# Kernel optimization log

Measured on AMD Instinct MI355X. Metric: run time of the kernel, lower is better.

The kernel has to match this reference:

```python
import jax, jax.numpy as jnp
import numpy as np
from jax import lax

D_MODEL = 1024
STATE_DIM = 512
BATCH = 4
SEQ_LEN = 8192


def _cayley_eigenvalues(a_params, n):
    # a_full = [0, a_1..a_half, -a_half-1..., antisymmetric tail]
    half = n // 2
    a_full = jnp.zeros((n,), dtype=a_params.dtype)
    a_full = a_full.at[1:half + 1].set(a_params)
    a_full = a_full.at[half + 1:].set(-a_params[::-1][: n - half - 1])
    a_hat = jnp.fft.fft(a_full)            # complex64
    omega = jnp.imag(a_hat)                # (n,), float32
    ones = jnp.ones_like(omega)
    num = lax.complex(ones, -omega)
    den = lax.complex(ones, omega)
    return num / den                        # (n,), |lambda|=1


def setup_inputs() -> dict:
    key = jax.random.key(0)
    k1, k2, k3, k4 = jax.random.split(key, 4)
    u = jax.random.normal(k1, (BATCH, SEQ_LEN, D_MODEL), dtype=jnp.float32)
    a_params = jax.random.normal(k2, (STATE_DIM // 2,), dtype=jnp.float32) * 0.1
    # torch Linear weights: B.weight (state_dim, d_model), C.weight (d_model, state_dim)
    B_w = jax.random.normal(k3, (STATE_DIM, D_MODEL), dtype=jnp.float32) / np.sqrt(D_MODEL)
    C_w = jax.random.normal(k4, (D_MODEL, STATE_DIM), dtype=jnp.float32) / np.sqrt(STATE_DIM)
    D = jnp.ones((D_MODEL,), dtype=jnp.float32)
    return {"u": u, "a_params": a_params, "B_w": B_w, "C_w": C_w, "D": D}


def reference(u, a_params, B_w, C_w, D):
    batch, seq_len, d = u.shape
    n = B_w.shape[0]
    # 1) input projection: (b, t, n)
    Bu = jnp.einsum("btd,nd->btn", u, B_w)
    # 2) per-channel geometric kernel k_j[t] = lambda_j^t
    eig = _cayley_eigenvalues(a_params, n)                 # (n,) complex64
    t = jnp.arange(seq_len, dtype=jnp.float32)
    kernel = jnp.exp(t[:, None] * jnp.log(eig)[None, :])   # (T, n) complex64
    # 3) causal convolution via FFT with next-pow2(2T) padding
    fft_len = 1
    while fft_len < 2 * seq_len:
        fft_len *= 2
    pad = fft_len - seq_len
    kernel_padded = jnp.pad(kernel, ((0, pad), (0, 0)))
    K_hat = jnp.fft.fft(kernel_padded, axis=0)             # (F, n)
    Bu_padded = jnp.pad(Bu, ((0, 0), (0, pad), (0, 0))).astype(jnp.complex64)
    Bu_hat = jnp.fft.fft(Bu_padded, axis=1)                # (b, F, n)
    h = jnp.fft.ifft(K_hat[None] * Bu_hat, axis=1).real[:, :seq_len, :]
    # 4) output projection + skip
    y = jnp.einsum("btn,dn->btd", h, C_w) + D * u
    return y
```

## Files before the change

kernel.cpp:

```cpp
#include <hip/hip_runtime.h>
#include <cstdint>
#include <cstddef>

#define D_MODEL   1024
#define STATE_DIM 512
#define BATCH     4
#define SEQ_LEN   8192
#define M_TOTAL   (BATCH * SEQ_LEN)

typedef unsigned short ushort_t;
typedef __attribute__((ext_vector_type(8))) __bf16 bf16x8;
typedef __attribute__((ext_vector_type(4))) float  f32x4;


__device__ inline ushort_t f2bf(float f) {
  union { float f; uint32_t u; } v; v.f = f;
  uint32_t u = v.u;
  uint32_t r = (u + 0x7FFFu + ((u >> 16) & 1u)) >> 16;
  return (ushort_t)r;
}

__device__ inline float bf2f(ushort_t b) {
  union { uint32_t u; float f; } v; v.u = ((uint32_t)b) << 16;
  return v.f;
}

__device__ inline void llds16(const void* g, void* l) {
  __builtin_amdgcn_global_load_lds(
      (__attribute__((address_space(1))) void*)(void*)g,
      (__attribute__((address_space(3))) void*)l,
      16, 0, 0);
}


__global__ void convert_f32_bf16(const float* __restrict__ in,
                                 ushort_t* __restrict__ out, int n4) {
  int i = blockIdx.x * blockDim.x + threadIdx.x;
  if (i >= n4) return;
  const float4 v = ((const float4*)in)[i];
  ushort4 o;
  o.x = f2bf(v.x); o.y = f2bf(v.y); o.z = f2bf(v.z); o.w = f2bf(v.w);
  ((ushort4*)out)[i] = o;
}


#define NCHUNK 128
#define CLEN   64
#define SOFF   (BATCH * NCHUNK * STATE_DIM)

__global__ __launch_bounds__(64)
void eigen_kernel(const float* __restrict__ a_params, float* __restrict__ lam) {
  const int k = blockIdx.x;
  const int l = threadIdx.x;
  const float c = 6.283185307179586f / 512.0f;
  float om = 0.f;
#pragma unroll
  for (int s = 0; s < 8; ++s) {
    const int n = s * 64 + l;
    float v = 0.f;
    if (n >= 1 && n <= STATE_DIM / 2)      v = a_params[n - 1];
    else if (n > STATE_DIM / 2)            v = -a_params[STATE_DIM - n];
    const int p = (k * n) & 511;
    om -= v * sinf(c * (float)p);
  }
#pragma unroll
  for (int off = 32; off; off >>= 1) om += __shfl_down(om, off);
  if (l == 0) {
    const float d  = 1.f / (1.f + om * om);
    const float lr = (1.f - om * om) * d;
    const float li = -2.f * om * d;
    double th = atan2((double)li, (double)lr) * (double)CLEN;
    lam[k]        = lr;
    lam[512 + k]  = li;
    lam[1024 + k] = (float)cos(th);
    lam[1536 + k] = (float)sin(th);
  }
}


template <int KDIM, int NDIM, bool OUT_BF16, bool FUSE_SKIP>
__global__ __launch_bounds__(256, 4)
void gemm_bt(const ushort_t* __restrict__ A,
             const ushort_t* __restrict__ Bw,
             void* __restrict__ outv,
             const ushort_t* __restrict__ skip_b,
             const float* __restrict__ Dvec) {
  __shared__ __align__(16) ushort_t smA[2 * 128 * 32];
  __shared__ __align__(16) ushort_t smB[2 * 128 * 32];
  const int tid    = threadIdx.x;
  const int wave   = tid >> 6, lane = tid & 63;
  const int lane16 = lane & 15, quad = lane >> 4;
  const int wm = (wave & 1) * 64, wn = (wave >> 1) * 64;
  const int row0 = blockIdx.x * 128;
  const int col0 = blockIdx.y * 128;

  f32x4 acc[4][4];
#pragma unroll
  for (int i = 0; i < 4; ++i)
#pragma unroll
    for (int j = 0; j < 4; ++j) {
      f32x4 z = {0.f, 0.f, 0.f, 0.f};
      acc[i][j] = z;
    }

  const int s_r0 = tid >> 2;
  const int s_c0 = (tid & 3) ^ ((s_r0 >> 1) & 3);
  const int s_r1 = (256 + tid) >> 2;
  const int s_c1 = (tid & 3) ^ ((s_r1 >> 1) & 3);
  const int o0 = (wave * 64) * 16;
  const int o1 = (256 + wave * 64) * 16;

  const ushort_t* gA0 = A  + (size_t)(row0 + s_r0) * KDIM + s_c0 * 8;
  const ushort_t* gB0 = Bw + (size_t)(col0 + s_r0) * KDIM + s_c0 * 8;
  const ushort_t* gA1 = A  + (size_t)(row0 + s_r1) * KDIM + s_c1 * 8;
  const ushort_t* gB1 = Bw + (size_t)(col0 + s_r1) * KDIM + s_c1 * 8;

#define STAGE(k0, buf)                                                   \
  do {                                                                   \
    char* bA = (char*)(smA + (buf) * (128 * 32));                        \
    char* bB = (char*)(smB + (buf) * (128 * 32));                        \
    llds16(gA0 + (k0), bA + o0);                                         \
    llds16(gB0 + (k0), bB + o0);                                         \
    llds16(gA1 + (k0), bA + o1);                                         \
    llds16(gB1 + (k0), bB + o1);                                         \
  } while (0)

  STAGE(0, 0);
  __syncthreads();

  constexpr int NIT = KDIM / 32;
  int cur = 0;
#pragma unroll 2
  for (int it = 0; it < NIT; ++it) {
    if (it + 1 < NIT) STAGE((it + 1) * 32, cur ^ 1);

    const ushort_t* sA = smA + cur * (128 * 32);
    const ushort_t* sB = smB + cur * (128 * 32);
    bf16x8 af[4], bfr[4];
#pragma unroll
    for (int mi = 0; mi < 4; ++mi) {
      const int m = wm + mi * 16 + lane16;
      const int pc = quad ^ ((m >> 1) & 3);
      af[mi] = *(const bf16x8*)(sA + (m * 4 + pc) * 8);
    }
#pragma unroll
    for (int ni = 0; ni < 4; ++ni) {
      const int n = wn + ni * 16 + lane16;
      const int pc = quad ^ ((n >> 1) & 3);
      bfr[ni] = *(const bf16x8*)(sB + (n * 4 + pc) * 8);
    }
#pragma unroll
    for (int mi = 0; mi < 4; ++mi)
#pragma unroll
      for (int ni = 0; ni < 4; ++ni)
        acc[mi][ni] = __builtin_amdgcn_mfma_f32_16x16x32_bf16(
            af[mi], bfr[ni], acc[mi][ni], 0, 0, 0);

    __syncthreads();
    cur ^= 1;
  }
#undef STAGE

#pragma unroll
  for (int mi = 0; mi < 4; ++mi) {
#pragma unroll
    for (int ni = 0; ni < 4; ++ni) {
      const int row = row0 + wm + mi * 16 + quad * 4;
      const int col = col0 + wn + ni * 16 + lane16;
      float dv = 0.f;
      if (FUSE_SKIP) dv = Dvec[col];
#pragma unroll
      for (int r = 0; r < 4; ++r) {
        const size_t o = (size_t)(row + r) * NDIM + col;
        float val = acc[mi][ni][r];
        if (FUSE_SKIP) val = fmaf(dv, bf2f(skip_b[o]), val);
        if (OUT_BF16) ((ushort_t*)outv)[o] = f2bf(val);
        else          ((float*)outv)[o] = val;
      }
    }
  }
}


__global__ __launch_bounds__(128)
void scan_chunks(const ushort_t* __restrict__ Bu, const float* __restrict__ lam,
                 float* __restrict__ S) {
  const int j = threadIdx.x * 4;
  const int c = blockIdx.x & (NCHUNK - 1);
  const int b = blockIdx.x >> 7;
  float lr[4], li[4], hr[4] = {0,0,0,0}, hi[4] = {0,0,0,0};
#pragma unroll
  for (int q = 0; q < 4; ++q) { lr[q] = lam[j + q]; li[q] = lam[512 + j + q]; }
  const ushort_t* p = Bu + ((size_t)(b * SEQ_LEN + c * CLEN)) * STATE_DIM + j;
#pragma unroll 4
  for (int t = 0; t < CLEN; ++t) {
    const ushort4 x4 = *(const ushort4*)(p + (size_t)t * STATE_DIM);
    const float x[4] = {bf2f(x4.x), bf2f(x4.y), bf2f(x4.z), bf2f(x4.w)};
#pragma unroll
    for (int q = 0; q < 4; ++q) {
      const float nr = fmaf(lr[q], hr[q], fmaf(-li[q], hi[q], x[q]));
      const float ni = fmaf(lr[q], hi[q], li[q] * hr[q]);
      hr[q] = nr; hi[q] = ni;
    }
  }
  const size_t o = (size_t)(b * NCHUNK + c) * STATE_DIM + j;
#pragma unroll
  for (int q = 0; q < 4; ++q) { S[o + q] = hr[q]; S[SOFF + o + q] = hi[q]; }
}

__global__ __launch_bounds__(512)
void scan_carry(const float* __restrict__ lam, const float* __restrict__ S,
                float* __restrict__ Hin) {
  const int idx = blockIdx.x * blockDim.x + threadIdx.x;
  const int j = idx & 511, b = idx >> 9;
  const float pr = lam[1024 + j], pi = lam[1536 + j];
  float cr = 0.f, ci = 0.f;
  for (int c = 0; c < NCHUNK; ++c) {
    const size_t o = (size_t)(b * NCHUNK + c) * STATE_DIM + j;
    Hin[o] = cr; Hin[SOFF + o] = ci;
    const float sr = S[o], si = S[SOFF + o];
    const float nr = fmaf(pr, cr, fmaf(-pi, ci, sr));
    const float ni = fmaf(pr, ci, fmaf(pi, cr, si));
    cr = nr; ci = ni;
  }
}

__global__ __launch_bounds__(128)
void scan_final(const ushort_t* __restrict__ Bu, const float* __restrict__ lam,
                const float* __restrict__ Hin, ushort_t* __restrict__ h) {
  const int j = threadIdx.x * 4;
  const int c = blockIdx.x & (NCHUNK - 1);
  const int b = blockIdx.x >> 7;
  float lr[4], li[4], hr[4], hi[4];
#pragma unroll
  for (int q = 0; q < 4; ++q) { lr[q] = lam[j + q]; li[q] = lam[512 + j + q]; }
  const size_t so = (size_t)(b * NCHUNK + c) * STATE_DIM + j;
#pragma unroll
  for (int q = 0; q < 4; ++q) { hr[q] = Hin[so + q]; hi[q] = Hin[SOFF + so + q]; }
  const size_t base = ((size_t)(b * SEQ_LEN + c * CLEN)) * STATE_DIM + j;
#pragma unroll 4
  for (int t = 0; t < CLEN; ++t) {
    const ushort4 x4 = *(const ushort4*)(Bu + base + (size_t)t * STATE_DIM);
    const float x[4] = {bf2f(x4.x), bf2f(x4.y), bf2f(x4.z), bf2f(x4.w)};
    ushort4 o4;
#pragma unroll
    for (int q = 0; q < 4; ++q) {
      const float nr = fmaf(lr[q], hr[q], fmaf(-li[q], hi[q], x[q]));
      const float ni = fmaf(lr[q], hi[q], li[q] * hr[q]);
      hr[q] = nr; hi[q] = ni;
    }
    o4.x = f2bf(hr[0]); o4.y = f2bf(hr[1]); o4.z = f2bf(hr[2]); o4.w = f2bf(hr[3]);
    *(ushort4*)(h + base + (size_t)t * STATE_DIM) = o4;
  }
}


extern "C" void kernel_launch(void* const* d_in, const int* in_sizes, int n_in,
                              void* d_out, int out_size, void* d_ws, size_t ws_size,
                              hipStream_t stream) {
  const float* u  = (const float*)d_in[0];
  const float* ap = (const float*)d_in[1];
  const float* Bw = (const float*)d_in[2];
  const float* Cw = (const float*)d_in[3];
  const float* Dv = (const float*)d_in[4];
  float* y = (float*)d_out;

  char* ws = (char*)d_ws;
  ushort_t* ub  = (ushort_t*)(ws + 0);
  ushort_t* bwb = (ushort_t*)(ws + 67108864);
  ushort_t* cwb = (ushort_t*)(ws + 68157440);
  float*    lam = (float*)   (ws + 69206016);
  ushort_t* Bu  = (ushort_t*)(ws + 69214208);
  ushort_t* hb  = (ushort_t*)(ws + 102768640);
  float*    S   = (float*)   (ws + 136323072);
  float*    Hin = (float*)   (ws + 138420224);

  convert_f32_bf16<<<32768, 256, 0, stream>>>(u,  ub,  (M_TOTAL * D_MODEL) / 4);
  convert_f32_bf16<<<512,   256, 0, stream>>>(Bw, bwb, (STATE_DIM * D_MODEL) / 4);
  convert_f32_bf16<<<512,   256, 0, stream>>>(Cw, cwb, (D_MODEL * STATE_DIM) / 4);
  eigen_kernel<<<512, 64, 0, stream>>>(ap, lam);

  gemm_bt<D_MODEL, STATE_DIM, true, false>
      <<<dim3(M_TOTAL / 128, STATE_DIM / 128), 256, 0, stream>>>(
          ub, bwb, Bu, nullptr, nullptr);

  scan_chunks<<<BATCH * NCHUNK, 128, 0, stream>>>(Bu, lam, S);
  scan_carry<<<BATCH, 512, 0, stream>>>(lam, S, Hin);
  scan_final<<<BATCH * NCHUNK, 128, 0, stream>>>(Bu, lam, Hin, hb);

  gemm_bt<STATE_DIM, D_MODEL, false, true>
      <<<dim3(M_TOTAL / 128, D_MODEL / 128), 256, 0, stream>>>(
          hb, cwb, y, ub, Dv);
}
```

Measured before the change: 376.7 us.

## Replace 128x128 GEMM with 256x256-tile 8-wave kernel with deep LDS pipelining

Both projection GEMMs now use 256x256 output tiles with 512 threads, 64-wide K steps and a 128KB double-buffered dynamic LDS buffer. Global-to-LDS loads for tile k+2 are interleaved with MFMA quadrants, using explicit barriers, setprio and vmcnt waits. Block IDs are remapped to group workgroups, likely for cache locality. The aim is more data reuse per tile and better overlap of memory traffic with matrix math, at the cost of lower occupancy and a large LDS footprint.

Measured after the change: 380.4 us. About the same (+1.0%).

```diff
diff --git a/kernel.cpp b/kernel.cpp
--- a/kernel.cpp
+++ b/kernel.cpp
@@ -78,95 +78,146 @@
 }
 
 
+template <int QM, int QN>
+__device__ __forceinline__ void mfma_quad(f32x4 (&acc)[8][4],
+                                          const bf16x8 (&a)[4][2],
+                                          const bf16x8 (&b)[2][2]) {
+#pragma unroll
+  for (int mi = 0; mi < 4; ++mi)
+#pragma unroll
+    for (int ni = 0; ni < 2; ++ni)
+#pragma unroll
+      for (int ks = 0; ks < 2; ++ks)
+        acc[QM * 4 + mi][QN * 2 + ni] = __builtin_amdgcn_mfma_f32_16x16x32_bf16(
+            a[mi][ks], b[ni][ks], acc[QM * 4 + mi][QN * 2 + ni], 0, 0, 0);
+}
+
+template <int NFR>
+__device__ __forceinline__ void load_frags(bf16x8 (&dst)[NFR][2], const char* base) {
+#pragma unroll
+  for (int i = 0; i < NFR; ++i)
+#pragma unroll
+    for (int ks = 0; ks < 2; ++ks)
+      dst[i][ks] = *(const bf16x8*)(base + i * 2048 + ks * 64);
+}
+
 template <int KDIM, int NDIM, bool OUT_BF16, bool FUSE_SKIP>
-__global__ __launch_bounds__(256, 4)
-void gemm_bt(const ushort_t* __restrict__ A,
+__global__ __launch_bounds__(512, 2)
+void gemm256(const ushort_t* __restrict__ A,
              const ushort_t* __restrict__ Bw,
              void* __restrict__ outv,
              const ushort_t* __restrict__ skip_b,
              const float* __restrict__ Dvec) {
-  __shared__ __align__(16) ushort_t smA[2 * 128 * 32];
-  __shared__ __align__(16) ushort_t smB[2 * 128 * 32];
+  extern __shared__ char sm[];
+  constexpr int NIT = KDIM / 64;
   const int tid    = threadIdx.x;
   const int wave   = tid >> 6, lane = tid & 63;
   const int lane16 = lane & 15, quad = lane >> 4;
-  const int wm = (wave & 1) * 64, wn = (wave >> 1) * 64;
-  const int row0 = blockIdx.x * 128;
-  const int col0 = blockIdx.y * 128;
-
-  f32x4 acc[4][4];
-#pragma unroll
-  for (int i = 0; i < 4; ++i)
+  const int wm = wave >> 2, wn = wave & 3;
+
+  const int gx   = gridDim.x;
+  const int nwg  = gx * gridDim.y;
+  const int bid0 = blockIdx.y * gx + blockIdx.x;
+  const int bid  = (bid0 & 7) * (nwg >> 3) + (bid0 >> 3);
+  const int row0 = (bid % gx) * 256;
+  const int col0 = (bid / gx) * 256;
+
+  const int xr     = ((lane16 >> 2) & 1) << 1;
+  const int lfrag  = lane16 * 128 + ((quad ^ xr) * 16);
+  const int aRegion = wm * 16384;
+  const int bRegion = 32768 + (wn >> 1) * 16384 + (wn & 1) * 8192;
+
+  const int srow = tid >> 3;
+  const int sck  = (tid & 7) ^ (((tid >> 5) & 1) << 1);
+  const ushort_t* gA = A  + (size_t)(row0 + srow) * KDIM + sck * 8;
+  const ushort_t* gB = Bw + (size_t)(col0 + srow) * KDIM + sck * 8;
+  char* ldsW = sm + wave * 1024;
+
+  f32x4 acc[8][4];
+#pragma unroll
+  for (int i = 0; i < 8; ++i)
 #pragma unroll
     for (int j = 0; j < 4; ++j) {
       f32x4 z = {0.f, 0.f, 0.f, 0.f};
       acc[i][j] = z;
     }
-
-  const int s_r0 = tid >> 2;
-  const int s_c0 = (tid & 3) ^ ((s_r0 >> 1) & 3);
-  const int s_r1 = (256 + tid) >> 2;
-  const int s_c1 = (tid & 3) ^ ((s_r1 >> 1) & 3);
-  const int o0 = (wave * 64) * 16;
-  const int o1 = (256 + wave * 64) * 16;
-
-  const ushort_t* gA0 = A  + (size_t)(row0 + s_r0) * KDIM + s_c0 * 8;
-  const ushort_t* gB0 = Bw + (size_t)(col0 + s_r0) * KDIM + s_c0 * 8;
-  const ushort_t* gA1 = A  + (size_t)(row0 + s_r1) * KDIM + s_c1 * 8;
-  const ushort_t* gB1 = Bw + (size_t)(col0 + s_r1) * KDIM + s_c1 * 8;
-
-#define STAGE(k0, buf)                                                   \
-  do {                                                                   \
-    char* bA = (char*)(smA + (buf) * (128 * 32));                        \
-    char* bB = (char*)(smB + (buf) * (128 * 32));                        \
-    llds16(gA0 + (k0), bA + o0);                                         \
-    llds16(gB0 + (k0), bB + o0);                                         \
-    llds16(gA1 + (k0), bA + o1);                                         \
-    llds16(gB1 + (k0), bB + o1);                                         \
+  bf16x8 af[4][2], b0[2][2], b1[2][2];
+
+#define STG(gbase, ktile, h, isB, s)                                          \
+  do {                                                                        \
+    const ushort_t* _g = (gbase) + (size_t)((h) * 128) * KDIM + (ktile) * 64; \
+    char* _l = ldsW + (s) * 65536 + (isB) * 32768 + (h) * 16384;              \
+    llds16(_g, _l);                                                           \
+    llds16(_g + (size_t)64 * KDIM, _l + 8192);                                \
   } while (0)
 
-  STAGE(0, 0);
-  __syncthreads();
-
-  constexpr int NIT = KDIM / 32;
-  int cur = 0;
-#pragma unroll 2
-  for (int it = 0; it < NIT; ++it) {
-    if (it + 1 < NIT) STAGE((it + 1) * 32, cur ^ 1);
-
-    const ushort_t* sA = smA + cur * (128 * 32);
-    const ushort_t* sB = smB + cur * (128 * 32);
-    bf16x8 af[4], bfr[4];
-#pragma unroll
-    for (int mi = 0; mi < 4; ++mi) {
-      const int m = wm + mi * 16 + lane16;
-      const int pc = quad ^ ((m >> 1) & 3);
-      af[mi] = *(const bf16x8*)(sA + (m * 4 + pc) * 8);
-    }
+#define BAR()                                                                 \
+  do {                                                                        \
+    __builtin_amdgcn_sched_barrier(0);                                        \
+    asm volatile("" ::: "memory");                                            \
+    __builtin_amdgcn_s_barrier();                                             \
+    asm volatile("" ::: "memory");                                            \
+    __builtin_amdgcn_sched_barrier(0);                                        \
+  } while (0)
+
+#define MQ(QM, QN, B)                                                         \
+  do {                                                                        \
+    __builtin_amdgcn_s_setprio(1);                                            \
+    mfma_quad<QM, QN>(acc, af, B);                                            \
+    __builtin_amdgcn_s_setprio(0);                                            \
+  } while (0)
+
+  STG(gA, 0, 0, 0, 0); STG(gA, 0, 1, 0, 0);
+  STG(gB, 0, 0, 1, 0); STG(gB, 0, 1, 1, 0);
+  STG(gA, 1, 0, 0, 1); STG(gA, 1, 1, 0, 1);
+  STG(gB, 1, 0, 1, 1); STG(gB, 1, 1, 1, 1);
+  asm volatile("s_waitcnt vmcnt(8)" ::: "memory");
+  BAR();
+
+#define KTILE(kt, s)                                                          \
+  do {                                                                        \
+                                                 \
+    load_frags<4>(af, sm + (s) * 65536 + aRegion + lfrag);                    \
+    load_frags<2>(b0, sm + (s) * 65536 + bRegion + lfrag);                    \
+    BAR();                                                                    \
+    MQ(0, 0, b0);                                                             \
+    BAR();                                                                    \
+                                                            \
+    load_frags<2>(b1, sm + (s) * 65536 + bRegion + 4096 + lfrag);             \
+    BAR();                                                                    \
+    MQ(0, 1, b1);                                                             \
+    BAR();                                                                    \
+                \
+    load_frags<4>(af, sm + (s) * 65536 + aRegion + 8192 + lfrag);             \
+    if ((kt) + 2 < NIT) { STG(gB, (kt) + 2, 0, 1, s); STG(gB, (kt) + 2, 1, 1, s); } \
+    BAR();                                                                    \
+    MQ(1, 1, b1);                                                             \
+    BAR();                                                                    \
+           \
+    if ((kt) + 2 < NIT) { STG(gA, (kt) + 2, 0, 0, s); STG(gA, (kt) + 2, 1, 0, s); } \
+    BAR();                                                                    \
+    MQ(1, 0, b0);                                                             \
+    if ((kt) + 2 < NIT)       asm volatile("s_waitcnt vmcnt(8)" ::: "memory"); \
+    else if ((kt) + 2 == NIT) asm volatile("s_waitcnt vmcnt(0)" ::: "memory"); \
+    BAR();                                                                    \
+  } while (0)
+
+#pragma unroll 1
+  for (int kt = 0; kt < NIT; kt += 2) {
+    KTILE(kt, 0);
+    KTILE(kt + 1, 1);
+  }
+#undef KTILE
+#undef MQ
+#undef BAR
+#undef STG
+
+#pragma unroll
+  for (int mi = 0; mi < 8; ++mi) {
 #pragma unroll
     for (int ni = 0; ni < 4; ++ni) {
-      const int n = wn + ni * 16 + lane16;
-      const int pc = quad ^ ((n >> 1) & 3);
-      bfr[ni] = *(const bf16x8*)(sB + (n * 4 + pc) * 8);
-    }
-#pragma unroll
-    for (int mi = 0; mi < 4; ++mi)
-#pragma unroll
-      for (int ni = 0; ni < 4; ++ni)
-        acc[mi][ni] = __builtin_amdgcn_mfma_f32_16x16x32_bf16(
-            af[mi], bfr[ni], acc[mi][ni], 0, 0, 0);
-
-    __syncthreads();
-    cur ^= 1;
-  }
-#undef STAGE
-
-#pragma unroll
-  for (int mi = 0; mi < 4; ++mi) {
-#pragma unroll
-    for (int ni = 0; ni < 4; ++ni) {
-      const int row = row0 + wm + mi * 16 + quad * 4;
-      const int col = col0 + wn + ni * 16 + lane16;
+      const int row = row0 + wm * 128 + mi * 16 + quad * 4;
+      const int col = col0 + wn * 64 + ni * 16 + lane16;
       float dv = 0.f;
       if (FUSE_SKIP) dv = Dvec[col];
 #pragma unroll
@@ -275,20 +326,31 @@
   float*    S   = (float*)   (ws + 136323072);
   float*    Hin = (float*)   (ws + 138420224);
 
+  static bool attr_done = false;
+  if (!attr_done) {
+    hipFuncSetAttribute(
+        reinterpret_cast<const void*>(&gemm256<D_MODEL, STATE_DIM, true, false>),
+        hipFuncAttributeMaxDynamicSharedMemorySize, 131072);
+    hipFuncSetAttribute(
+        reinterpret_cast<const void*>(&gemm256<STATE_DIM, D_MODEL, false, true>),
+        hipFuncAttributeMaxDynamicSharedMemorySize, 131072);
+    attr_done = true;
+  }
+
   convert_f32_bf16<<<32768, 256, 0, stream>>>(u,  ub,  (M_TOTAL * D_MODEL) / 4);
   convert_f32_bf16<<<512,   256, 0, stream>>>(Bw, bwb, (STATE_DIM * D_MODEL) / 4);
   convert_f32_bf16<<<512,   256, 0, stream>>>(Cw, cwb, (D_MODEL * STATE_DIM) / 4);
   eigen_kernel<<<512, 64, 0, stream>>>(ap, lam);
 
-  gemm_bt<D_MODEL, STATE_DIM, true, false>
-      <<<dim3(M_TOTAL / 128, STATE_DIM / 128), 256, 0, stream>>>(
+  gemm256<D_MODEL, STATE_DIM, true, false>
+      <<<dim3(M_TOTAL / 256, STATE_DIM / 256), 512, 131072, stream>>>(
           ub, bwb, Bu, nullptr, nullptr);
 
   scan_chunks<<<BATCH * NCHUNK, 128, 0, stream>>>(Bu, lam, S);
   scan_carry<<<BATCH, 512, 0, stream>>>(lam, S, Hin);
   scan_final<<<BATCH * NCHUNK, 128, 0, stream>>>(Bu, lam, Hin, hb);
 
-  gemm_bt<STATE_DIM, D_MODEL, false, true>
-      <<<dim3(M_TOTAL / 128, D_MODEL / 128), 256, 0, stream>>>(
+  gemm256<STATE_DIM, D_MODEL, false, true>
+      <<<dim3(M_TOTAL / 256, D_MODEL / 256), 512, 131072, stream>>>(
           hb, cwb, y, ub, Dv);
 }
```

## Fuse fp32-to-bf16 conversion of input into first GEMM and read fp32 skip

Applied to the files above, without the earlier changes.

Removes the separate conversion pass over the large input tensor. The first projection GEMM now loads fp32 activations into LDS and converts them to bf16 when building MFMA fragments. The output GEMM reads the skip term directly from the fp32 input. This cuts a full read/write pass, but it doubles the A-tile LDS footprint, lowers the occupancy target, and doubles skip-read bytes.

Measured after the change: 410.6 us. 9.0% more time.

```diff
diff --git a/kernel.cpp b/kernel.cpp
--- a/kernel.cpp
+++ b/kernel.cpp
@@ -78,13 +78,120 @@
 }
 
 
-template <int KDIM, int NDIM, bool OUT_BF16, bool FUSE_SKIP>
+__global__ __launch_bounds__(256, 3)
+void gemm_a32(const float* __restrict__ A,
+              const ushort_t* __restrict__ Bw,
+              ushort_t* __restrict__ out) {
+  constexpr int KDIM = D_MODEL, NDIM = STATE_DIM, NIT = KDIM / 32;
+  __shared__ __align__(16) float    smA[2 * 128 * 32];
+  __shared__ __align__(16) ushort_t smB[2 * 128 * 32];
+  const int tid    = threadIdx.x;
+  const int wave   = tid >> 6, lane = tid & 63;
+  const int lane16 = lane & 15, quad = lane >> 4;
+  const int wm = (wave & 1) * 64, wn = (wave >> 1) * 64;
+  const int row0 = blockIdx.x * 128;
+  const int col0 = blockIdx.y * 128;
+
+  f32x4 acc[4][4];
+#pragma unroll
+  for (int i = 0; i < 4; ++i)
+#pragma unroll
+    for (int j = 0; j < 4; ++j) {
+      f32x4 z = {0.f, 0.f, 0.f, 0.f};
+      acc[i][j] = z;
+    }
+
+  const float* gA[4];
+#pragma unroll
+  for (int j = 0; j < 4; ++j) {
+    const int r = wave * 32 + j * 8 + (lane >> 3);
+    const int c = (lane & 7) ^ (((j & 1) << 2) | (lane >> 4));
+    gA[j] = A + (size_t)(row0 + r) * KDIM + c * 4;
+  }
+  const int s_r0 = tid >> 2;
+  const int s_c0 = (tid & 3) ^ ((s_r0 >> 1) & 3);
+  const int s_r1 = 64 + s_r0;
+  const int s_c1 = (tid & 3) ^ ((s_r1 >> 1) & 3);
+  const ushort_t* gB0 = Bw + (size_t)(col0 + s_r0) * KDIM + s_c0 * 8;
+  const ushort_t* gB1 = Bw + (size_t)(col0 + s_r1) * KDIM + s_c1 * 8;
+  const int ob0 = wave * 1024, ob1 = 4096 + wave * 1024;
+
+#define STAGE(itk, buf)                                                  \
+  do {                                                                   \
+    char* bA = (char*)(smA + (buf) * (128 * 32));                        \
+    char* bB = (char*)(smB + (buf) * (128 * 32));                        \
+    llds16(gA[0] + (itk) * 32, bA + (wave * 32 + 0) * 128);              \
+    llds16(gA[1] + (itk) * 32, bA + (wave * 32 + 8) * 128);              \
+    llds16(gA[2] + (itk) * 32, bA + (wave * 32 + 16) * 128);             \
+    llds16(gA[3] + (itk) * 32, bA + (wave * 32 + 24) * 128);             \
+    llds16(gB0 + (itk) * 32, bB + ob0);                                  \
+    llds16(gB1 + (itk) * 32, bB + ob1);                                  \
+  } while (0)
+
+  STAGE(0, 0);
+  __syncthreads();
+
+  int cur = 0;
+#pragma unroll 2
+  for (int it = 0; it < NIT; ++it) {
+    if (it + 1 < NIT) STAGE(it + 1, cur ^ 1);
+
+    const float*    sA = smA + cur * (128 * 32);
+    const ushort_t* sB = smB + cur * (128 * 32);
+    bf16x8 af[4], bfr[4];
+    const int pA = lane16 >> 1;
+#pragma unroll
+    for (int mi = 0; mi < 4; ++mi) {
+      const int m = wm + mi * 16 + lane16;
+      const char* base = (const char*)sA + m * 128;
+      const f32x4 lo = *(const f32x4*)(base + (((2 * quad)     ^ pA) << 4));
+      const f32x4 hi = *(const f32x4*)(base + (((2 * quad + 1) ^ pA) << 4));
+      bf16x8 a;
+#pragma unroll
+      for (int i = 0; i < 4; ++i) { a[i] = (__bf16)lo[i]; a[4 + i] = (__bf16)hi[i]; }
+      af[mi] = a;
+    }
+#pragma unroll
+    for (int ni = 0; ni < 4; ++ni) {
+      const int n = wn + ni * 16 + lane16;
+      const int pc = quad ^ ((n >> 1) & 3);
+      bfr[ni] = *(const bf16x8*)(sB + (n * 4 + pc) * 8);
+    }
+#pragma unroll
+    for (int mi = 0; mi < 4; ++mi)
+#pragma unroll
+      for (int ni = 0; ni < 4; ++ni)
+        acc[mi][ni] = __builtin_amdgcn_mfma_f32_16x16x32_bf16(
+            af[mi], bfr[ni], acc[mi][ni], 0, 0, 0);
+
+    __syncthreads();
+    cur ^= 1;
+  }
+#undef STAGE
+
+#pragma unroll
+  for (int mi = 0; mi < 4; ++mi) {
+#pragma unroll
+    for (int ni = 0; ni < 4; ++ni) {
+      const int row = row0 + wm + mi * 16 + quad * 4;
+      const int col = col0 + wn + ni * 16 + lane16;
+#pragma unroll
+      for (int r = 0; r < 4; ++r) {
+        const size_t o = (size_t)(row + r) * NDIM + col;
+        out[o] = f2bf(acc[mi][ni][r]);
+      }
+    }
+  }
+}
+
+
 __global__ __launch_bounds__(256, 4)
-void gemm_bt(const ushort_t* __restrict__ A,
-             const ushort_t* __restrict__ Bw,
-             void* __restrict__ outv,
-             const ushort_t* __restrict__ skip_b,
-             const float* __restrict__ Dvec) {
+void gemm2(const ushort_t* __restrict__ A,
+           const ushort_t* __restrict__ Bw,
+           float* __restrict__ out,
+           const float* __restrict__ skip_f,
+           const float* __restrict__ Dvec) {
+  constexpr int KDIM = STATE_DIM, NDIM = D_MODEL, NIT = KDIM / 32;
   __shared__ __align__(16) ushort_t smA[2 * 128 * 32];
   __shared__ __align__(16) ushort_t smB[2 * 128 * 32];
   const int tid    = threadIdx.x;
@@ -105,7 +212,7 @@
 
   const int s_r0 = tid >> 2;
   const int s_c0 = (tid & 3) ^ ((s_r0 >> 1) & 3);
-  const int s_r1 = (256 + tid) >> 2;
+  const int s_r1 = 64 + s_r0;
   const int s_c1 = (tid & 3) ^ ((s_r1 >> 1) & 3);
   const int o0 = (wave * 64) * 16;
   const int o1 = (256 + wave * 64) * 16;
@@ -128,7 +235,6 @@
   STAGE(0, 0);
   __syncthreads();
 
-  constexpr int NIT = KDIM / 32;
   int cur = 0;
 #pragma unroll 2
   for (int it = 0; it < NIT; ++it) {
@@ -167,15 +273,11 @@
     for (int ni = 0; ni < 4; ++ni) {
       const int row = row0 + wm + mi * 16 + quad * 4;
       const int col = col0 + wn + ni * 16 + lane16;
-      float dv = 0.f;
-      if (FUSE_SKIP) dv = Dvec[col];
+      const float dv = Dvec[col];
 #pragma unroll
       for (int r = 0; r < 4; ++r) {
         const size_t o = (size_t)(row + r) * NDIM + col;
-        float val = acc[mi][ni][r];
-        if (FUSE_SKIP) val = fmaf(dv, bf2f(skip_b[o]), val);
-        if (OUT_BF16) ((ushort_t*)outv)[o] = f2bf(val);
-        else          ((float*)outv)[o] = val;
+        out[o] = fmaf(dv, skip_f[o], acc[mi][ni][r]);
       }
     }
   }
@@ -266,29 +368,25 @@
   float* y = (float*)d_out;
 
   char* ws = (char*)d_ws;
-  ushort_t* ub  = (ushort_t*)(ws + 0);
-  ushort_t* bwb = (ushort_t*)(ws + 67108864);
-  ushort_t* cwb = (ushort_t*)(ws + 68157440);
-  float*    lam = (float*)   (ws + 69206016);
-  ushort_t* Bu  = (ushort_t*)(ws + 69214208);
-  ushort_t* hb  = (ushort_t*)(ws + 102768640);
-  float*    S   = (float*)   (ws + 136323072);
-  float*    Hin = (float*)   (ws + 138420224);
-
-  convert_f32_bf16<<<32768, 256, 0, stream>>>(u,  ub,  (M_TOTAL * D_MODEL) / 4);
-  convert_f32_bf16<<<512,   256, 0, stream>>>(Bw, bwb, (STATE_DIM * D_MODEL) / 4);
-  convert_f32_bf16<<<512,   256, 0, stream>>>(Cw, cwb, (D_MODEL * STATE_DIM) / 4);
+  ushort_t* bwb = (ushort_t*)(ws + 0);
+  ushort_t* cwb = (ushort_t*)(ws + 1048576);
+  float*    lam = (float*)   (ws + 2097152);
+  ushort_t* Bu  = (ushort_t*)(ws + 2105344);
+  ushort_t* hb  = (ushort_t*)(ws + 35659776);
+  float*    S   = (float*)   (ws + 69214208);
+  float*    Hin = (float*)   (ws + 71311360);
+
+  convert_f32_bf16<<<512, 256, 0, stream>>>(Bw, bwb, (STATE_DIM * D_MODEL) / 4);
+  convert_f32_bf16<<<512, 256, 0, stream>>>(Cw, cwb, (D_MODEL * STATE_DIM) / 4);
   eigen_kernel<<<512, 64, 0, stream>>>(ap, lam);
 
-  gemm_bt<D_MODEL, STATE_DIM, true, false>
-      <<<dim3(M_TOTAL / 128, STATE_DIM / 128), 256, 0, stream>>>(
-          ub, bwb, Bu, nullptr, nullptr);
+  gemm_a32<<<dim3(M_TOTAL / 128, STATE_DIM / 128), 256, 0, stream>>>(
+      u, bwb, Bu);
 
   scan_chunks<<<BATCH * NCHUNK, 128, 0, stream>>>(Bu, lam, S);
   scan_carry<<<BATCH, 512, 0, stream>>>(lam, S, Hin);
   scan_final<<<BATCH * NCHUNK, 128, 0, stream>>>(Bu, lam, Hin, hb);
 
-  gemm_bt<STATE_DIM, D_MODEL, false, true>
-      <<<dim3(M_TOTAL / 128, D_MODEL / 128), 256, 0, stream>>>(
-          hb, cwb, y, ub, Dv);
-}
+  gemm2<<<dim3(M_TOTAL / 128, D_MODEL / 128), 256, 0, stream>>>(
+      hb, cwb, y, u, Dv);
+}
```

## Shrink GEMM block tile to 64x128 with two waves per block

Applied to the files above, without the earlier changes.

Both projection GEMMs now use 128-thread blocks (two waves), each computing a 64x128 output tile, instead of 256-thread blocks computing 128x128. Staging and the swizzle indexing are reworked so each wave loads 16-row slices of A and B into shared memory. The grid doubles along M, which gives more blocks and less shared memory per block. The cost is less reuse of each B tile and more redundant global loads of B across blocks.

After: 401.1 us. 6.5% more time.

```diff
diff --git a/kernel.cpp b/kernel.cpp
--- a/kernel.cpp
+++ b/kernel.cpp
@@ -79,19 +79,19 @@
 
 
 template <int KDIM, int NDIM, bool OUT_BF16, bool FUSE_SKIP>
-__global__ __launch_bounds__(256, 4)
+__global__ __launch_bounds__(128, 3)
 void gemm_bt(const ushort_t* __restrict__ A,
              const ushort_t* __restrict__ Bw,
              void* __restrict__ outv,
              const ushort_t* __restrict__ skip_b,
              const float* __restrict__ Dvec) {
-  __shared__ __align__(16) ushort_t smA[2 * 128 * 32];
+  __shared__ __align__(16) ushort_t smA[2 * 64 * 32];
   __shared__ __align__(16) ushort_t smB[2 * 128 * 32];
   const int tid    = threadIdx.x;
   const int wave   = tid >> 6, lane = tid & 63;
   const int lane16 = lane & 15, quad = lane >> 4;
-  const int wm = (wave & 1) * 64, wn = (wave >> 1) * 64;
-  const int row0 = blockIdx.x * 128;
+  const int wn = wave * 64;
+  const int row0 = blockIdx.x * 64;
   const int col0 = blockIdx.y * 128;
 
   f32x4 acc[4][4];
@@ -103,26 +103,28 @@
       acc[i][j] = z;
     }
 
-  const int s_r0 = tid >> 2;
-  const int s_c0 = (tid & 3) ^ ((s_r0 >> 1) & 3);
-  const int s_r1 = (256 + tid) >> 2;
-  const int s_c1 = (tid & 3) ^ ((s_r1 >> 1) & 3);
-  const int o0 = (wave * 64) * 16;
-  const int o1 = (256 + wave * 64) * 16;
-
-  const ushort_t* gA0 = A  + (size_t)(row0 + s_r0) * KDIM + s_c0 * 8;
-  const ushort_t* gB0 = Bw + (size_t)(col0 + s_r0) * KDIM + s_c0 * 8;
-  const ushort_t* gA1 = A  + (size_t)(row0 + s_r1) * KDIM + s_c1 * 8;
-  const ushort_t* gB1 = Bw + (size_t)(col0 + s_r1) * KDIM + s_c1 * 8;
+  const int srow = lane >> 2;
+  const int sck  = (lane & 3) ^ ((lane >> 3) & 3);
+  const ushort_t* gA0 = A  + (size_t)(row0 +      wave * 16 + srow) * KDIM + sck * 8;
+  const ushort_t* gA1 = A  + (size_t)(row0 + 32 + wave * 16 + srow) * KDIM + sck * 8;
+  const ushort_t* gB0 = Bw + (size_t)(col0 +      wave * 16 + srow) * KDIM + sck * 8;
+  const ushort_t* gB1 = Bw + (size_t)(col0 + 32 + wave * 16 + srow) * KDIM + sck * 8;
+  const ushort_t* gB2 = Bw + (size_t)(col0 + 64 + wave * 16 + srow) * KDIM + sck * 8;
+  const ushort_t* gB3 = Bw + (size_t)(col0 + 96 + wave * 16 + srow) * KDIM + sck * 8;
+  const int oA0 = (wave * 16) * 64,      oA1 = (32 + wave * 16) * 64;
+  const int oB0 = (wave * 16) * 64,      oB1 = (32 + wave * 16) * 64;
+  const int oB2 = (64 + wave * 16) * 64, oB3 = (96 + wave * 16) * 64;
 
 #define STAGE(k0, buf)                                                   \
   do {                                                                   \
-    char* bA = (char*)(smA + (buf) * (128 * 32));                        \
+    char* bA = (char*)(smA + (buf) * (64 * 32));                         \
     char* bB = (char*)(smB + (buf) * (128 * 32));                        \
-    llds16(gA0 + (k0), bA + o0);                                         \
-    llds16(gB0 + (k0), bB + o0);                                         \
-    llds16(gA1 + (k0), bA + o1);                                         \
-    llds16(gB1 + (k0), bB + o1);                                         \
+    llds16(gA0 + (k0), bA + oA0);                                        \
+    llds16(gA1 + (k0), bA + oA1);                                        \
+    llds16(gB0 + (k0), bB + oB0);                                        \
+    llds16(gB1 + (k0), bB + oB1);                                        \
+    llds16(gB2 + (k0), bB + oB2);                                        \
+    llds16(gB3 + (k0), bB + oB3);                                        \
   } while (0)
 
   STAGE(0, 0);
@@ -134,19 +136,18 @@
   for (int it = 0; it < NIT; ++it) {
     if (it + 1 < NIT) STAGE((it + 1) * 32, cur ^ 1);
 
-    const ushort_t* sA = smA + cur * (128 * 32);
+    const ushort_t* sA = smA + cur * (64 * 32);
     const ushort_t* sB = smB + cur * (128 * 32);
     bf16x8 af[4], bfr[4];
+    const int pc = quad ^ ((lane16 >> 1) & 3);
 #pragma unroll
     for (int mi = 0; mi < 4; ++mi) {
-      const int m = wm + mi * 16 + lane16;
-      const int pc = quad ^ ((m >> 1) & 3);
+      const int m = mi * 16 + lane16;
       af[mi] = *(const bf16x8*)(sA + (m * 4 + pc) * 8);
     }
 #pragma unroll
     for (int ni = 0; ni < 4; ++ni) {
       const int n = wn + ni * 16 + lane16;
-      const int pc = quad ^ ((n >> 1) & 3);
       bfr[ni] = *(const bf16x8*)(sB + (n * 4 + pc) * 8);
     }
 #pragma unroll
@@ -165,7 +166,7 @@
   for (int mi = 0; mi < 4; ++mi) {
 #pragma unroll
     for (int ni = 0; ni < 4; ++ni) {
-      const int row = row0 + wm + mi * 16 + quad * 4;
+      const int row = row0 + mi * 16 + quad * 4;
       const int col = col0 + wn + ni * 16 + lane16;
       float dv = 0.f;
       if (FUSE_SKIP) dv = Dvec[col];
@@ -281,7 +282,7 @@
   eigen_kernel<<<512, 64, 0, stream>>>(ap, lam);
 
   gemm_bt<D_MODEL, STATE_DIM, true, false>
-      <<<dim3(M_TOTAL / 128, STATE_DIM / 128), 256, 0, stream>>>(
+      <<<dim3(M_TOTAL / 64, STATE_DIM / 128), 128, 0, stream>>>(
           ub, bwb, Bu, nullptr, nullptr);
 
   scan_chunks<<<BATCH * NCHUNK, 128, 0, stream>>>(Bu, lam, S);
@@ -289,6 +290,6 @@
   scan_final<<<BATCH * NCHUNK, 128, 0, stream>>>(Bu, lam, Hin, hb);
 
   gemm_bt<STATE_DIM, D_MODEL, false, true>
-      <<<dim3(M_TOTAL / 128, D_MODEL / 128), 256, 0, stream>>>(
+      <<<dim3(M_TOTAL / 64, D_MODEL / 128), 128, 0, stream>>>(
           hb, cwb, y, ub, Dv);
 }
```
